# Optimization experiments

Measured on AMD Instinct MI355X. Metric: run time of the kernel, lower is better.

Reference implementation:

```python
import jax, jax.numpy as jnp
from jax import lax
import numpy as np

B, T, C = 32, 2048, 512
CLAMP_LO, CLAMP_HI = 1e-4, 1.0 - 1e-4


def setup_inputs() -> dict:
    key = jax.random.key(0)
    x = jax.random.normal(key, (B, T, C), dtype=jnp.float32)
    # parameter initialized at logit(0.9), repeated per channel
    logit_alpha = jnp.full((C,), float(np.log(0.9 / 0.1)), dtype=jnp.float32)
    delta = jnp.asarray(1.0, dtype=jnp.float32)
    return {"x": x, "logit_alpha": logit_alpha, "delta": delta}


def reference(x, logit_alpha, delta):
    # x: [B, T, C]; logit_alpha: [C]; delta: scalar
    a = jnp.clip(jax.nn.sigmoid(logit_alpha), CLAMP_LO, CLAMP_HI).astype(x.dtype)  # [C]
    one_minus_a = 1.0 - a  # [C], broadcasts over [B, C]
    d = delta.astype(x.dtype)

    def step(y_prev, x_t):  # y_prev, x_t: [B, C]
        r = x_t - y_prev
        g = jnp.where(jnp.abs(r) <= d, r, d * jnp.sign(r))  # Huber gradient
        y = y_prev + one_minus_a * g
        return y, y

    y0 = x[:, 0, :]  # [B, C]
    xs = jnp.swapaxes(x[:, 1:, :], 0, 1)  # [T-1, B, C]
    _, ys = lax.scan(step, y0, xs)  # ys: [T-1, B, C]
    y = jnp.concatenate([y0[None], ys], axis=0)  # [T, B, C]
    return jnp.swapaxes(y, 0, 1)  # [B, T, C]
```

## Files before the change

### kernel.cpp

```cpp
#include <hip/hip_runtime.h>
#include <math.h>


#define TT   2048
#define CC   512
#define TILE 64
#define NTIL (TT / TILE)

__global__ __launch_bounds__(64, 1)
void huber_ema_kernel(const float* __restrict__ x,
                      const float* __restrict__ logit_alpha,
                      const float* __restrict__ delta,
                      float* __restrict__ y)
{
    const int blk  = blockIdx.x;
    const int b    = blk >> 3;
    const int cc   = blk & 7;
    const int lane = threadIdx.x;

    const float la = logit_alpha[(cc << 6) + lane];
    float a = 1.0f / (1.0f + expf(-la));
    a = fminf(fmaxf(a, 1e-4f), 1.0f - 1e-4f);
    const float oma = 1.0f - a;
    const float d = delta[0];

    const float* __restrict__ xb = x + (size_t)b * TT * CC + (cc << 6);
    float*       __restrict__ yb = y + (size_t)b * TT * CC + (cc << 6);

    const int tl = lane >> 4;
    const int c4 = (lane & 15) << 2;
    const float* __restrict__ xl = xb + (size_t)tl * CC + c4;
    float*       __restrict__ yl = yb + (size_t)tl * CC + c4;

    __shared__ float xs[2][TILE * 64];
    __shared__ float ys[2][TILE * 64];

    float4 xr[16];

    float yv = xb[lane];

    {
        float4 t0[16];
        #pragma unroll
        for (int g = 0; g < 16; ++g)
            t0[g] = *(const float4*)(xl + (size_t)(g * 4) * CC);
        #pragma unroll
        for (int g = 0; g < 16; ++g)
            *(float4*)&xs[0][g * 256 + (lane << 2)] = t0[g];
    }
    #pragma unroll
    for (int g = 0; g < 16; ++g)
        xr[g] = *(const float4*)(xl + (size_t)(TILE + g * 4) * CC);

    for (int k = 0; k < NTIL; ++k) {
        const float* __restrict__ bx  = xs[k & 1];
        float*       __restrict__ bxn = xs[(k + 1) & 1];
        float*       __restrict__ by  = ys[k & 1];

        float xin[TILE];
        #pragma unroll
        for (int i = 0; i < TILE; ++i)
            xin[i] = bx[i * 64 + lane];
        __builtin_amdgcn_sched_barrier(0);

        if (k + 1 < NTIL) {
            #pragma unroll
            for (int g = 0; g < 16; ++g)
                *(float4*)&bxn[g * 256 + (lane << 2)] = xr[g];
        }
        if (k + 2 < NTIL) {
            #pragma unroll
            for (int g = 0; g < 16; ++g)
                xr[g] = *(const float4*)(xl + (size_t)((k + 2) * TILE + g * 4) * CC);
        }
        __builtin_amdgcn_sched_barrier(0);

        #pragma unroll
        for (int i = 0; i < TILE; ++i) {
            float r = xin[i] - yv;
            yv += oma * fminf(fmaxf(r, -d), d);
            by[i * 64 + lane] = yv;
        }
        __builtin_amdgcn_sched_barrier(0);

        const size_t tb = (size_t)k * TILE;
        #pragma unroll
        for (int g = 0; g < 16; ++g) {
            float4 v = *(const float4*)&by[g * 256 + (lane << 2)];
            *(float4*)(yl + (tb + (size_t)(g * 4)) * CC) = v;
        }
    }
}

extern "C" void kernel_launch(void* const* d_in, const int* in_sizes, int n_in,
                              void* d_out, int out_size, void* d_ws, size_t ws_size,
                              hipStream_t stream) {
    const float* x  = (const float*)d_in[0];
    const float* la = (const float*)d_in[1];
    const float* dl = (const float*)d_in[2];
    float* y = (float*)d_out;

    huber_ema_kernel<<<dim3(256), dim3(64), 0, stream>>>(x, la, dl, y);
}
```

Measured before the change: 268.1 us.

## Use async global-to-LDS loads with a 4-deep ring buffer and vmcnt waits

Replaces the register-staged double buffer with direct global_load_lds transfers into a four-slot LDS ring, gated by explicit s_waitcnt vmcnt counts. Tiles shrink to 32 timesteps so more loads can be in flight ahead of the serial scan while register pressure drops. The aim is to hide global memory latency behind the sequential recurrence with only 256 single-wave blocks. It relies on hand-counted vmcnt values that include the outstanding stores, so a miscount could cause stalls or races.

Result: no change. 271.3 us (+1.2%).

```diff
diff --git a/kernel.cpp b/kernel.cpp
--- a/kernel.cpp
+++ b/kernel.cpp
@@ -4,8 +4,63 @@
 
 #define TT   2048
 #define CC   512
-#define TILE 64
+#define TILE 32
 #define NTIL (TT / TILE)
+#define LPT  8
+#define RING 4
+
+__device__ __forceinline__ void async16(const float* g, float* l) {
+    __builtin_amdgcn_global_load_lds(
+        (const __attribute__((address_space(1))) void*)g,
+        (__attribute__((address_space(3))) void*)l, 16, 0, 0);
+}
+
+template<int N> __device__ __forceinline__ void vm_wait() {
+    if constexpr (N == 24) asm volatile("s_waitcnt vmcnt(24)" ::: "memory");
+    else if constexpr (N == 32) asm volatile("s_waitcnt vmcnt(32)" ::: "memory");
+    else if constexpr (N == 40) asm volatile("s_waitcnt vmcnt(40)" ::: "memory");
+    else if constexpr (N == 48) asm volatile("s_waitcnt vmcnt(48)" ::: "memory");
+    else                        asm volatile("s_waitcnt vmcnt(0)"  ::: "memory");
+    __builtin_amdgcn_sched_barrier(0);
+}
+
+template<int WAITN, bool PF>
+__device__ __forceinline__ void tile_body(int k, const float* __restrict__ xl,
+                                          float* __restrict__ yl,
+                                          float* __restrict__ xslot,
+                                          float* __restrict__ ysb,
+                                          float& yv, float oma, float d, int lane)
+{
+    vm_wait<WAITN>();
+
+    float xin[TILE];
+    #pragma unroll
+    for (int i = 0; i < TILE; ++i) xin[i] = xslot[i * 64 + lane];
+    __builtin_amdgcn_sched_barrier(0);
+
+    #pragma unroll
+    for (int i = 0; i < TILE; ++i) {
+        float r = xin[i] - yv;
+        yv += oma * fminf(fmaxf(r, -d), d);
+        ysb[i * 64 + lane] = yv;
+    }
+    __builtin_amdgcn_sched_barrier(0);
+
+    #pragma unroll
+    for (int g = 0; g < LPT; ++g) {
+        float4 v = *(const float4*)&ysb[g * 256 + (lane << 2)];
+        *(float4*)(yl + (size_t)(k * TILE + g * 4) * CC) = v;
+    }
+    __builtin_amdgcn_sched_barrier(0);
+
+    if (PF) {
+        #pragma unroll
+        for (int g = 0; g < LPT; ++g)
+            async16(xl + (size_t)((k + RING) * TILE + g * 4) * CC,
+                    &xslot[g * 256]);
+    }
+    __builtin_amdgcn_sched_barrier(0);
+}
 
 __global__ __launch_bounds__(64, 1)
 void huber_ema_kernel(const float* __restrict__ x,
@@ -18,78 +73,40 @@
     const int cc   = blk & 7;
     const int lane = threadIdx.x;
 
+    __shared__ float xs[RING][TILE * 64];
+    __shared__ float ys[TILE * 64];
+
     const float la = logit_alpha[(cc << 6) + lane];
+    const float d  = delta[0];
+    const float* __restrict__ xb = x + (size_t)b * TT * CC + (cc << 6);
+    float*       __restrict__ yb = y + (size_t)b * TT * CC + (cc << 6);
+    float yv = xb[lane];
+
     float a = 1.0f / (1.0f + expf(-la));
     a = fminf(fmaxf(a, 1e-4f), 1.0f - 1e-4f);
     const float oma = 1.0f - a;
-    const float d = delta[0];
 
-    const float* __restrict__ xb = x + (size_t)b * TT * CC + (cc << 6);
-    float*       __restrict__ yb = y + (size_t)b * TT * CC + (cc << 6);
+    const float* __restrict__ xl = xb + (size_t)(lane >> 4) * CC + ((lane & 15) << 2);
+    float*       __restrict__ yl = yb + (size_t)(lane >> 4) * CC + ((lane & 15) << 2);
 
-    const int tl = lane >> 4;
-    const int c4 = (lane & 15) << 2;
-    const float* __restrict__ xl = xb + (size_t)tl * CC + c4;
-    float*       __restrict__ yl = yb + (size_t)tl * CC + c4;
+    #pragma unroll
+    for (int t = 0; t < RING; ++t) {
+        #pragma unroll
+        for (int g = 0; g < LPT; ++g)
+            async16(xl + (size_t)(t * TILE + g * 4) * CC, &xs[t][g * 256]);
+    }
 
-    __shared__ float xs[2][TILE * 64];
-    __shared__ float ys[2][TILE * 64];
+    tile_body<24, true >(0, xl, yl, xs[0], ys, yv, oma, d, lane);
+    tile_body<32, true >(1, xl, yl, xs[1], ys, yv, oma, d, lane);
+    tile_body<40, true >(2, xl, yl, xs[2], ys, yv, oma, d, lane);
 
-    float4 xr[16];
+    for (int k = 3; k <= NTIL - 5; ++k)
+        tile_body<48, true >(k, xl, yl, xs[k & 3], ys, yv, oma, d, lane);
 
-    float yv = xb[lane];
-
-    {
-        float4 t0[16];
-        #pragma unroll
-        for (int g = 0; g < 16; ++g)
-            t0[g] = *(const float4*)(xl + (size_t)(g * 4) * CC);
-        #pragma unroll
-        for (int g = 0; g < 16; ++g)
-            *(float4*)&xs[0][g * 256 + (lane << 2)] = t0[g];
-    }
-    #pragma unroll
-    for (int g = 0; g < 16; ++g)
-        xr[g] = *(const float4*)(xl + (size_t)(TILE + g * 4) * CC);
-
-    for (int k = 0; k < NTIL; ++k) {
-        const float* __restrict__ bx  = xs[k & 1];
-        float*       __restrict__ bxn = xs[(k + 1) & 1];
-        float*       __restrict__ by  = ys[k & 1];
-
-        float xin[TILE];
-        #pragma unroll
-        for (int i = 0; i < TILE; ++i)
-            xin[i] = bx[i * 64 + lane];
-        __builtin_amdgcn_sched_barrier(0);
-
-        if (k + 1 < NTIL) {
-            #pragma unroll
-            for (int g = 0; g < 16; ++g)
-                *(float4*)&bxn[g * 256 + (lane << 2)] = xr[g];
-        }
-        if (k + 2 < NTIL) {
-            #pragma unroll
-            for (int g = 0; g < 16; ++g)
-                xr[g] = *(const float4*)(xl + (size_t)((k + 2) * TILE + g * 4) * CC);
-        }
-        __builtin_amdgcn_sched_barrier(0);
-
-        #pragma unroll
-        for (int i = 0; i < TILE; ++i) {
-            float r = xin[i] - yv;
-            yv += oma * fminf(fmaxf(r, -d), d);
-            by[i * 64 + lane] = yv;
-        }
-        __builtin_amdgcn_sched_barrier(0);
-
-        const size_t tb = (size_t)k * TILE;
-        #pragma unroll
-        for (int g = 0; g < 16; ++g) {
-            float4 v = *(const float4*)&by[g * 256 + (lane << 2)];
-            *(float4*)(yl + (tb + (size_t)(g * 4)) * CC) = v;
-        }
-    }
+    tile_body<48, false>(NTIL - 4, xl, yl, xs[(NTIL - 4) & 3], ys, yv, oma, d, lane);
+    tile_body<40, false>(NTIL - 3, xl, yl, xs[(NTIL - 3) & 3], ys, yv, oma, d, lane);
+    tile_body<32, false>(NTIL - 2, xl, yl, xs[(NTIL - 2) & 3], ys, yv, oma, d, lane);
+    tile_body<24, false>(NTIL - 1, xl, yl, xs[(NTIL - 1) & 3], ys, yv, oma, d, lane);
 }
 
 extern "C" void kernel_launch(void* const* d_in, const int* in_sizes, int n_in,
```
